# Kernel optimization log

Measured on AMD Instinct MI355X. Metric: run time of the kernel, lower is better.

## Reference

```python
import jax, jax.numpy as jnp
import numpy as np

N_WIRES = 4
DIM = 1 << N_WIRES  # 16
N_PATCH = 14 * 14   # 196


def _random_unitary_16(seed=0):
    # Deterministic surrogate for tq.RandomLayer(n_ops=8): a fixed random
    # real orthogonal 16x16 operator applied to the 4-qubit state.
    rng = np.random.default_rng(seed)
    q, _ = np.linalg.qr(rng.standard_normal((DIM, DIM)))
    return jnp.asarray(q, dtype=jnp.float32)


def _linear_params(rng, fan_in, fan_out):
    bound = 1.0 / np.sqrt(fan_in)
    w = rng.uniform(-bound, bound, size=(fan_out, fan_in)).astype(np.float32)
    b = rng.uniform(-bound, bound, size=(fan_out,)).astype(np.float32)
    return jnp.asarray(w), jnp.asarray(b)


def setup_inputs() -> dict:
    key = jax.random.key(0)
    x = jax.random.normal(key, (8192, 784), dtype=jnp.float32)
    rng = np.random.default_rng(1)
    fc1_w, fc1_b = _linear_params(rng, 784, 120)
    fc2_w, fc2_b = _linear_params(rng, 120, 84)
    fc3_w, fc3_b = _linear_params(rng, 84, 1)
    return {
        "x": x,
        "U": _random_unitary_16(),
        "fc1_w": fc1_w, "fc1_b": fc1_b,
        "fc2_w": fc2_w, "fc2_b": fc2_b,
        "fc3_w": fc3_w, "fc3_b": fc3_b,
    }


def _quantum_filter(x, U):
    # x: [b, 784] -> 2x2 patches in row-major order, per-patch wire data
    # [x[r,c], x[r,c+1], x[r+1,c], x[r+1,c+1]]
    b = x.shape[0]
    xp = x.reshape(b, 14, 2, 14, 2).transpose(0, 1, 3, 2, 4).reshape(b, N_PATCH, N_WIRES)
    # Encoder: RY(theta_w) on wire w starting from |0000> -> product state
    c = jnp.cos(0.5 * xp)  # [b, p, 4]
    s = jnp.sin(0.5 * xp)
    a = jnp.stack([c, s], axis=-1)  # [b, p, 4, 2] per-wire amplitudes
    psi = jnp.einsum("bpi,bpj,bpk,bpl->bpijkl",
                     a[:, :, 0], a[:, :, 1], a[:, :, 2], a[:, :, 3])
    psi = psi.reshape(b, N_PATCH, DIM)  # wire 0 = most significant bit
    # Fixed random layer (16x16 unitary)
    psi = jnp.einsum("ij,bpj->bpi", U, psi)
    # PauliZ expectation per wire: sum_i |psi_i|^2 * (1 - 2*bit_w(i))
    idx = jnp.arange(DIM)
    bits = (idx[:, None] >> (N_WIRES - 1 - jnp.arange(N_WIRES))) & 1  # [16, 4]
    zsign = (1 - 2 * bits).astype(psi.dtype)
    meas = jnp.einsum("bpi,iw->bpw", psi * psi, zsign)  # [b, p, 4]
    return meas.reshape(b, N_PATCH * N_WIRES)  # [b, 784]


def reference(x, U, fc1_w, fc1_b, fc2_w, fc2_b, fc3_w, fc3_b):
    feats = _quantum_filter(x, U)
    h = jax.nn.relu(feats @ fc1_w.T + fc1_b)
    h = jax.nn.relu(h @ fc2_w.T + fc2_b)
    logits = (h @ fc3_w.T + fc3_b)[:, 0]  # [b], matches inputs.squeeze()
    # = P(|1>) = (1 + sin(theta)) / 2 (analytic, shot-noise-free)
    exp_val = 0.5 * (1.0 + jnp.sin(logits))
    p = jax.nn.sigmoid(exp_val)
    return jnp.concatenate([p, 1.0 - p], axis=-1)  # [2*b], matches torch.cat on 1-D
```

## Files before the change

kernel.cpp:

```cpp
#include <hip/hip_runtime.h>
#include <hip/hip_bf16.h>
#include <math.h>


#define BATCH   8192
#define NPATCH  196
#define KPAD    800

typedef __attribute__((ext_vector_type(8))) short bfrag;
typedef __attribute__((ext_vector_type(4))) float f32x4;

static __device__ __forceinline__ unsigned short f2bf(float f) {
    __hip_bfloat16 h = __float2bfloat16(f);
    return __builtin_bit_cast(unsigned short, h);
}

__global__ __launch_bounds__(256) void qfilter_kernel(
    const float* __restrict__ x, const float* __restrict__ U,
    unsigned short* __restrict__ featsB)
{
    int gid = blockIdx.x * 256 + threadIdx.x;
    if (gid >= BATCH * NPATCH) return;
    int b = gid / NPATCH;
    int p = gid - b * NPATCH;
    int pr = p / 14;
    int pc = p - pr * 14;
    const float* xr = x + b * 784 + pr * 56 + pc * 2;
    float x0 = xr[0], x1 = xr[1], x2 = xr[28], x3 = xr[29];

    float s0, c0, s1, c1, s2, c2, s3, c3;
    __sincosf(0.5f * x0, &s0, &c0);
    __sincosf(0.5f * x1, &s1, &c1);
    __sincosf(0.5f * x2, &s2, &c2);
    __sincosf(0.5f * x3, &s3, &c3);

    float t01[4] = {c0 * c1, c0 * s1, s0 * c1, s0 * s1};
    float t23[4] = {c2 * c3, c2 * s3, s2 * c3, s2 * s3};
    float psi[16];
#pragma unroll
    for (int i = 0; i < 16; ++i) psi[i] = t01[i >> 2] * t23[i & 3];

    float m0 = 0.f, m1 = 0.f, m2 = 0.f, m3 = 0.f;
#pragma unroll
    for (int i = 0; i < 16; ++i) {
        float acc = 0.f;
#pragma unroll
        for (int j = 0; j < 16; ++j)
            acc = fmaf(U[i * 16 + j], psi[j], acc);
        float q = acc * acc;
        m0 += (i & 8) ? -q : q;
        m1 += (i & 4) ? -q : q;
        m2 += (i & 2) ? -q : q;
        m3 += (i & 1) ? -q : q;
    }
    ushort4 o;
    o.x = f2bf(m0); o.y = f2bf(m1); o.z = f2bf(m2); o.w = f2bf(m3);
    *reinterpret_cast<ushort4*>(featsB + (size_t)b * KPAD + p * 4) = o;

    if (p == 0) {
        uint4 z = {0u, 0u, 0u, 0u};
        *reinterpret_cast<uint4*>(featsB + (size_t)b * KPAD + 784) = z;
        *reinterpret_cast<uint4*>(featsB + (size_t)b * KPAD + 792) = z;
    }
}

__global__ __launch_bounds__(256) void w1prep_kernel(
    const float* __restrict__ w1, unsigned short* __restrict__ w1B)
{
    int t = blockIdx.x * 256 + threadIdx.x;
    if (t >= 128 * KPAD) return;
    int n = t / KPAD;
    int k = t - n * KPAD;
    float v = (n < 120 && k < 784) ? w1[n * 784 + k] : 0.f;
    w1B[t] = f2bf(v);
}

__global__ __launch_bounds__(64) void fc1_mfma_kernel(
    const unsigned short* __restrict__ featsB,
    const unsigned short* __restrict__ w1B,
    const float* __restrict__ b1, float* __restrict__ h1)
{
    int bid = blockIdx.x;
    int swz = (bid & 7) * 128 + (bid >> 3);
    int m0  = (swz >> 1) * 16;
    int nh  = swz & 1;
    int l   = threadIdx.x;
    int row = l & 15;
    int grp = l >> 4;

    const unsigned short* aptr = featsB + (size_t)(m0 + row) * KPAD + grp * 8;
    const unsigned short* bptr = w1B + (size_t)(nh * 64 + row) * KPAD + grp * 8;

    f32x4 acc0 = {}, acc1 = {}, acc2 = {}, acc3 = {};
    for (int k0 = 0; k0 < KPAD; k0 += 32) {
        bfrag a = *reinterpret_cast<const bfrag*>(aptr + k0);
        bfrag b0 = *reinterpret_cast<const bfrag*>(bptr + 0 * 16 * KPAD + k0);
        bfrag b1f = *reinterpret_cast<const bfrag*>(bptr + 1 * 16 * KPAD + k0);
        bfrag b2 = *reinterpret_cast<const bfrag*>(bptr + 2 * 16 * KPAD + k0);
        bfrag b3 = *reinterpret_cast<const bfrag*>(bptr + 3 * 16 * KPAD + k0);
        acc0 = __builtin_amdgcn_mfma_f32_16x16x32_bf16(a, b0, acc0, 0, 0, 0);
        acc1 = __builtin_amdgcn_mfma_f32_16x16x32_bf16(a, b1f, acc1, 0, 0, 0);
        acc2 = __builtin_amdgcn_mfma_f32_16x16x32_bf16(a, b2, acc2, 0, 0, 0);
        acc3 = __builtin_amdgcn_mfma_f32_16x16x32_bf16(a, b3, acc3, 0, 0, 0);
    }

    f32x4 accs[4] = {acc0, acc1, acc2, acc3};
#pragma unroll
    for (int nj = 0; nj < 4; ++nj) {
        int col = nh * 64 + nj * 16 + row;
        if (col < 120) {
            float bias = b1[col];
#pragma unroll
            for (int r = 0; r < 4; ++r) {
                float v = accs[nj][r] + bias;
                h1[(size_t)(m0 + grp * 4 + r) * 120 + col] = fmaxf(v, 0.f);
            }
        }
    }
}

__global__ __launch_bounds__(256) void head_kernel(
    const float* __restrict__ h1, const float* __restrict__ w2,
    const float* __restrict__ b2, const float* __restrict__ w3,
    const float* __restrict__ b3, float* __restrict__ out)
{
    __shared__ float h1s[64 * 120];
    __shared__ float w2s[84 * 120];
    __shared__ float h2s[64 * 84];
    const int tid = threadIdx.x;
    const int m0  = blockIdx.x * 64;

    for (int t = tid; t < 1920; t += 256) {
        *reinterpret_cast<float4*>(&h1s[t * 4]) =
            *reinterpret_cast<const float4*>(h1 + (size_t)m0 * 120 + t * 4);
    }
    for (int t = tid; t < 2520; t += 256) {
        *reinterpret_cast<float4*>(&w2s[t * 4]) =
            *reinterpret_cast<const float4*>(w2 + t * 4);
    }
    __syncthreads();

    for (int e = tid; e < 1344; e += 256) {
        int r  = e / 21;
        int nq = e - r * 21;
        int n0 = nq * 4;
        float4 bias = *reinterpret_cast<const float4*>(b2 + n0);
        float accv[4] = {bias.x, bias.y, bias.z, bias.w};
#pragma unroll
        for (int kq = 0; kq < 30; ++kq) {
            float4 a = *reinterpret_cast<const float4*>(&h1s[r * 120 + kq * 4]);
#pragma unroll
            for (int nn = 0; nn < 4; ++nn) {
                float4 wv = *reinterpret_cast<const float4*>(
                    &w2s[(n0 + nn) * 120 + kq * 4]);
                accv[nn] = fmaf(a.x, wv.x, accv[nn]);
                accv[nn] = fmaf(a.y, wv.y, accv[nn]);
                accv[nn] = fmaf(a.z, wv.z, accv[nn]);
                accv[nn] = fmaf(a.w, wv.w, accv[nn]);
            }
        }
        float4 o;
        o.x = fmaxf(accv[0], 0.f);
        o.y = fmaxf(accv[1], 0.f);
        o.z = fmaxf(accv[2], 0.f);
        o.w = fmaxf(accv[3], 0.f);
        *reinterpret_cast<float4*>(&h2s[r * 84 + n0]) = o;
    }
    __syncthreads();

    if (tid < 64) {
        int r = tid;
        float acc = b3[0];
#pragma unroll
        for (int kq = 0; kq < 21; ++kq) {
            float4 a  = *reinterpret_cast<const float4*>(&h2s[r * 84 + kq * 4]);
            float4 wv = *reinterpret_cast<const float4*>(w3 + kq * 4);
            acc = fmaf(a.x, wv.x, acc);
            acc = fmaf(a.y, wv.y, acc);
            acc = fmaf(a.z, wv.z, acc);
            acc = fmaf(a.w, wv.w, acc);
        }
        float ev = 0.5f * (1.0f + __sinf(acc));
        float pp = 1.0f / (1.0f + __expf(-ev));
        out[m0 + r]        = pp;
        out[8192 + m0 + r] = 1.0f - pp;
    }
}

extern "C" void kernel_launch(void* const* d_in, const int* in_sizes, int n_in,
                              void* d_out, int out_size, void* d_ws, size_t ws_size,
                              hipStream_t stream)
{
    (void)in_sizes; (void)n_in; (void)out_size; (void)ws_size;
    const float* x  = (const float*)d_in[0];
    const float* U  = (const float*)d_in[1];
    const float* w1 = (const float*)d_in[2];
    const float* b1 = (const float*)d_in[3];
    const float* w2 = (const float*)d_in[4];
    const float* b2 = (const float*)d_in[5];
    const float* w3 = (const float*)d_in[6];
    const float* b3 = (const float*)d_in[7];
    float* out = (float*)d_out;

    unsigned short* featsB = (unsigned short*)d_ws;
    unsigned short* w1B = featsB + (size_t)BATCH * KPAD;
    float* h1 = (float*)(w1B + (size_t)128 * KPAD);

    w1prep_kernel<<<dim3((128 * KPAD + 255) / 256), dim3(256), 0, stream>>>(w1, w1B);
    qfilter_kernel<<<dim3((BATCH * NPATCH) / 256), dim3(256), 0, stream>>>(x, U, featsB);
    fc1_mfma_kernel<<<dim3(1024), dim3(64), 0, stream>>>(featsB, w1B, b1, h1);
    head_kernel<<<dim3(BATCH / 64), dim3(256), 0, stream>>>(h1, w2, b2, w3, b3, out);
}
```

Measured before the change: 143.0 us.

## Fuse quantum filter, fc1 MFMA and head into one per-16-row kernel

Merges the quantum filter, the fc1 MFMA GEMM and the fc2/fc3 head into a single kernel in which each block handles 16 batch rows and keeps the bf16 features and h1 in shared memory. This removes the global round-trips for featsB and h1 and two kernel launches. The filter math is rewritten with float2 packed operations and a butterfly-style reduction for the Z expectations. In exchange, w2 is now read from global memory or cache inside the inner loop instead of being staged in LDS, and fc1 uses only two MFMA tiles per wave over a small 16-row M tile.

```diff
diff --git a/kernel.cpp b/kernel.cpp
--- a/kernel.cpp
+++ b/kernel.cpp
@@ -6,62 +6,16 @@
 #define BATCH   8192
 #define NPATCH  196
 #define KPAD    800
+#define FLD     808
+#define H1LD    132
 
 typedef __attribute__((ext_vector_type(8))) short bfrag;
 typedef __attribute__((ext_vector_type(4))) float f32x4;
+typedef __attribute__((ext_vector_type(2))) float f32x2;
 
 static __device__ __forceinline__ unsigned short f2bf(float f) {
     __hip_bfloat16 h = __float2bfloat16(f);
     return __builtin_bit_cast(unsigned short, h);
-}
-
-__global__ __launch_bounds__(256) void qfilter_kernel(
-    const float* __restrict__ x, const float* __restrict__ U,
-    unsigned short* __restrict__ featsB)
-{
-    int gid = blockIdx.x * 256 + threadIdx.x;
-    if (gid >= BATCH * NPATCH) return;
-    int b = gid / NPATCH;
-    int p = gid - b * NPATCH;
-    int pr = p / 14;
-    int pc = p - pr * 14;
-    const float* xr = x + b * 784 + pr * 56 + pc * 2;
-    float x0 = xr[0], x1 = xr[1], x2 = xr[28], x3 = xr[29];
-
-    float s0, c0, s1, c1, s2, c2, s3, c3;
-    __sincosf(0.5f * x0, &s0, &c0);
-    __sincosf(0.5f * x1, &s1, &c1);
-    __sincosf(0.5f * x2, &s2, &c2);
-    __sincosf(0.5f * x3, &s3, &c3);
-
-    float t01[4] = {c0 * c1, c0 * s1, s0 * c1, s0 * s1};
-    float t23[4] = {c2 * c3, c2 * s3, s2 * c3, s2 * s3};
-    float psi[16];
-#pragma unroll
-    for (int i = 0; i < 16; ++i) psi[i] = t01[i >> 2] * t23[i & 3];
-
-    float m0 = 0.f, m1 = 0.f, m2 = 0.f, m3 = 0.f;
-#pragma unroll
-    for (int i = 0; i < 16; ++i) {
-        float acc = 0.f;
-#pragma unroll
-        for (int j = 0; j < 16; ++j)
-            acc = fmaf(U[i * 16 + j], psi[j], acc);
-        float q = acc * acc;
-        m0 += (i & 8) ? -q : q;
-        m1 += (i & 4) ? -q : q;
-        m2 += (i & 2) ? -q : q;
-        m3 += (i & 1) ? -q : q;
-    }
-    ushort4 o;
-    o.x = f2bf(m0); o.y = f2bf(m1); o.z = f2bf(m2); o.w = f2bf(m3);
-    *reinterpret_cast<ushort4*>(featsB + (size_t)b * KPAD + p * 4) = o;
-
-    if (p == 0) {
-        uint4 z = {0u, 0u, 0u, 0u};
-        *reinterpret_cast<uint4*>(featsB + (size_t)b * KPAD + 784) = z;
-        *reinterpret_cast<uint4*>(featsB + (size_t)b * KPAD + 792) = z;
-    }
 }
 
 __global__ __launch_bounds__(256) void w1prep_kernel(
@@ -75,72 +29,123 @@
     w1B[t] = f2bf(v);
 }
 
-__global__ __launch_bounds__(64) void fc1_mfma_kernel(
-    const unsigned short* __restrict__ featsB,
+__global__ __launch_bounds__(256) void mega_kernel(
+    const float* __restrict__ x, const float* __restrict__ U,
     const unsigned short* __restrict__ w1B,
-    const float* __restrict__ b1, float* __restrict__ h1)
+    const float* __restrict__ b1,
+    const float* __restrict__ w2, const float* __restrict__ b2,
+    const float* __restrict__ w3, const float* __restrict__ b3,
+    float* __restrict__ out)
 {
-    int bid = blockIdx.x;
-    int swz = (bid & 7) * 128 + (bid >> 3);
-    int m0  = (swz >> 1) * 16;
-    int nh  = swz & 1;
-    int l   = threadIdx.x;
-    int row = l & 15;
-    int grp = l >> 4;
-
-    const unsigned short* aptr = featsB + (size_t)(m0 + row) * KPAD + grp * 8;
-    const unsigned short* bptr = w1B + (size_t)(nh * 64 + row) * KPAD + grp * 8;
-
-    f32x4 acc0 = {}, acc1 = {}, acc2 = {}, acc3 = {};
-    for (int k0 = 0; k0 < KPAD; k0 += 32) {
-        bfrag a = *reinterpret_cast<const bfrag*>(aptr + k0);
-        bfrag b0 = *reinterpret_cast<const bfrag*>(bptr + 0 * 16 * KPAD + k0);
-        bfrag b1f = *reinterpret_cast<const bfrag*>(bptr + 1 * 16 * KPAD + k0);
-        bfrag b2 = *reinterpret_cast<const bfrag*>(bptr + 2 * 16 * KPAD + k0);
-        bfrag b3 = *reinterpret_cast<const bfrag*>(bptr + 3 * 16 * KPAD + k0);
-        acc0 = __builtin_amdgcn_mfma_f32_16x16x32_bf16(a, b0, acc0, 0, 0, 0);
-        acc1 = __builtin_amdgcn_mfma_f32_16x16x32_bf16(a, b1f, acc1, 0, 0, 0);
-        acc2 = __builtin_amdgcn_mfma_f32_16x16x32_bf16(a, b2, acc2, 0, 0, 0);
-        acc3 = __builtin_amdgcn_mfma_f32_16x16x32_bf16(a, b3, acc3, 0, 0, 0);
-    }
-
-    f32x4 accs[4] = {acc0, acc1, acc2, acc3};
-#pragma unroll
-    for (int nj = 0; nj < 4; ++nj) {
-        int col = nh * 64 + nj * 16 + row;
-        if (col < 120) {
-            float bias = b1[col];
-#pragma unroll
-            for (int r = 0; r < 4; ++r) {
-                float v = accs[nj][r] + bias;
-                h1[(size_t)(m0 + grp * 4 + r) * 120 + col] = fmaxf(v, 0.f);
+    __shared__ unsigned short featsL[16 * FLD];
+    __shared__ float h1L[16 * H1LD];
+    __shared__ float h2L[16 * 84];
+
+    const int tid = threadIdx.x;
+    const int m0  = blockIdx.x * 16;
+
+    {
+        int r = tid >> 4;
+        int c = 784 + (tid & 15);
+        featsL[r * FLD + c] = 0;
+    }
+
+    const f32x2* U2 = reinterpret_cast<const f32x2*>(U);
+    for (int e = tid; e < 16 * NPATCH; e += 256) {
+        int r = e / NPATCH;
+        int p = e - r * NPATCH;
+        int pr = p / 14;
+        int pc = p - pr * 14;
+        const float* xr = x + (size_t)(m0 + r) * 784 + pr * 56 + pc * 2;
+        f32x2 xa = *reinterpret_cast<const f32x2*>(xr);
+        f32x2 xb = *reinterpret_cast<const f32x2*>(xr + 28);
+
+        float s0, c0, s1, c1, s2, c2, s3, c3;
+        __sincosf(0.5f * xa.x, &s0, &c0);
+        __sincosf(0.5f * xa.y, &s1, &c1);
+        __sincosf(0.5f * xb.x, &s2, &c2);
+        __sincosf(0.5f * xb.y, &s3, &c3);
+
+        float t01[4] = {c0 * c1, c0 * s1, s0 * c1, s0 * s1};
+        f32x2 t23p0 = {c2 * c3, c2 * s3};
+        f32x2 t23p1 = {s2 * c3, s2 * s3};
+
+        f32x2 psi2[8];
+#pragma unroll
+        for (int j = 0; j < 8; ++j)
+            psi2[j] = ((j & 1) ? t23p1 : t23p0) * t01[j >> 1];
+
+        f32x2 q2[8];
+#pragma unroll
+        for (int jq = 0; jq < 8; ++jq) {
+            f32x2 accA = U2[(2 * jq) * 8] * psi2[0];
+            f32x2 accB = U2[(2 * jq + 1) * 8] * psi2[0];
+#pragma unroll
+            for (int j = 1; j < 8; ++j) {
+                accA = U2[(2 * jq) * 8 + j] * psi2[j] + accA;
+                accB = U2[(2 * jq + 1) * 8 + j] * psi2[j] + accB;
             }
-        }
-    }
-}
-
-__global__ __launch_bounds__(256) void head_kernel(
-    const float* __restrict__ h1, const float* __restrict__ w2,
-    const float* __restrict__ b2, const float* __restrict__ w3,
-    const float* __restrict__ b3, float* __restrict__ out)
-{
-    __shared__ float h1s[64 * 120];
-    __shared__ float w2s[84 * 120];
-    __shared__ float h2s[64 * 84];
-    const int tid = threadIdx.x;
-    const int m0  = blockIdx.x * 64;
-
-    for (int t = tid; t < 1920; t += 256) {
-        *reinterpret_cast<float4*>(&h1s[t * 4]) =
-            *reinterpret_cast<const float4*>(h1 + (size_t)m0 * 120 + t * 4);
-    }
-    for (int t = tid; t < 2520; t += 256) {
-        *reinterpret_cast<float4*>(&w2s[t * 4]) =
-            *reinterpret_cast<const float4*>(w2 + t * 4);
+            float pa = accA.x + accA.y;
+            float pb = accB.x + accB.y;
+            f32x2 ph = {pa, pb};
+            q2[jq] = ph * ph;
+        }
+
+        f32x2 s01 = q2[0] + q2[1], s23 = q2[2] + q2[3];
+        f32x2 s45 = q2[4] + q2[5], s67 = q2[6] + q2[7];
+        f32x2 e0 = s01 + s23, e1 = s45 + s67;
+        f32x2 t0 = s01 - s23, t1 = s45 - s67;
+        f32x2 g  = (q2[0] - q2[1]) + (q2[2] - q2[3])
+                 + (q2[4] - q2[5]) + (q2[6] - q2[7]);
+        f32x2 F  = e0 + e1;
+        float m0v = (e0.x + e0.y) - (e1.x + e1.y);
+        float m1v = (t0.x + t0.y) + (t1.x + t1.y);
+        float m2v = g.x + g.y;
+        float m3v = F.x - F.y;
+
+        ushort4 o;
+        o.x = f2bf(m0v); o.y = f2bf(m1v); o.z = f2bf(m2v); o.w = f2bf(m3v);
+        *reinterpret_cast<ushort4*>(&featsL[r * FLD + p * 4]) = o;
     }
     __syncthreads();
 
-    for (int e = tid; e < 1344; e += 256) {
+    {
+        const int wave = tid >> 6;
+        const int lane = tid & 63;
+        const int row  = lane & 15;
+        const int grp  = lane >> 4;
+
+        const unsigned short* fA = &featsL[row * FLD + grp * 8];
+        const unsigned short* bp0 =
+            w1B + (size_t)(wave * 32 + row) * KPAD + grp * 8;
+        const unsigned short* bp1 = bp0 + 16 * KPAD;
+
+        f32x4 acc0 = {}, acc1 = {};
+        for (int k0 = 0; k0 < KPAD; k0 += 32) {
+            bfrag a  = *reinterpret_cast<const bfrag*>(fA + k0);
+            bfrag b0 = *reinterpret_cast<const bfrag*>(bp0 + k0);
+            bfrag b1f = *reinterpret_cast<const bfrag*>(bp1 + k0);
+            acc0 = __builtin_amdgcn_mfma_f32_16x16x32_bf16(a, b0, acc0, 0, 0, 0);
+            acc1 = __builtin_amdgcn_mfma_f32_16x16x32_bf16(a, b1f, acc1, 0, 0, 0);
+        }
+
+        f32x4 accs[2] = {acc0, acc1};
+#pragma unroll
+        for (int nj = 0; nj < 2; ++nj) {
+            int col = wave * 32 + nj * 16 + row;
+            if (col < 120) {
+                float bias = b1[col];
+#pragma unroll
+                for (int rr = 0; rr < 4; ++rr) {
+                    float v = accs[nj][rr] + bias;
+                    h1L[(grp * 4 + rr) * H1LD + col] = fmaxf(v, 0.f);
+                }
+            }
+        }
+    }
+    __syncthreads();
+
+    for (int e = tid; e < 16 * 21; e += 256) {
         int r  = e / 21;
         int nq = e - r * 21;
         int n0 = nq * 4;
@@ -148,11 +153,11 @@
         float accv[4] = {bias.x, bias.y, bias.z, bias.w};
 #pragma unroll
         for (int kq = 0; kq < 30; ++kq) {
-            float4 a = *reinterpret_cast<const float4*>(&h1s[r * 120 + kq * 4]);
+            float4 a = *reinterpret_cast<const float4*>(&h1L[r * H1LD + kq * 4]);
 #pragma unroll
             for (int nn = 0; nn < 4; ++nn) {
-                float4 wv = *reinterpret_cast<const float4*>(
-                    &w2s[(n0 + nn) * 120 + kq * 4]);
+                const float4 wv = *reinterpret_cast<const float4*>(
+                    w2 + (size_t)(n0 + nn) * 120 + kq * 4);
                 accv[nn] = fmaf(a.x, wv.x, accv[nn]);
                 accv[nn] = fmaf(a.y, wv.y, accv[nn]);
                 accv[nn] = fmaf(a.z, wv.z, accv[nn]);
@@ -164,16 +169,16 @@
         o.y = fmaxf(accv[1], 0.f);
         o.z = fmaxf(accv[2], 0.f);
         o.w = fmaxf(accv[3], 0.f);
-        *reinterpret_cast<float4*>(&h2s[r * 84 + n0]) = o;
+        *reinterpret_cast<float4*>(&h2L[r * 84 + n0]) = o;
     }
     __syncthreads();
 
-    if (tid < 64) {
+    if (tid < 16) {
         int r = tid;
         float acc = b3[0];
 #pragma unroll
         for (int kq = 0; kq < 21; ++kq) {
-            float4 a  = *reinterpret_cast<const float4*>(&h2s[r * 84 + kq * 4]);
+            float4 a  = *reinterpret_cast<const float4*>(&h2L[r * 84 + kq * 4]);
             float4 wv = *reinterpret_cast<const float4*>(w3 + kq * 4);
             acc = fmaf(a.x, wv.x, acc);
             acc = fmaf(a.y, wv.y, acc);
@@ -182,8 +187,8 @@
         }
         float ev = 0.5f * (1.0f + __sinf(acc));
         float pp = 1.0f / (1.0f + __expf(-ev));
-        out[m0 + r]        = pp;
-        out[8192 + m0 + r] = 1.0f - pp;
+        out[m0 + r]         = pp;
+        out[BATCH + m0 + r] = 1.0f - pp;
     }
 }
 
@@ -202,12 +207,9 @@
     const float* b3 = (const float*)d_in[7];
     float* out = (float*)d_out;
 
-    unsigned short* featsB = (unsigned short*)d_ws;
-    unsigned short* w1B = featsB + (size_t)BATCH * KPAD;
-    float* h1 = (float*)(w1B + (size_t)128 * KPAD);
+    unsigned short* w1B = (unsigned short*)d_ws;
 
     w1prep_kernel<<<dim3((128 * KPAD + 255) / 256), dim3(256), 0, stream>>>(w1, w1B);
-    qfilter_kernel<<<dim3((BATCH * NPATCH) / 256), dim3(256), 0, stream>>>(x, U, featsB);
-    fc1_mfma_kernel<<<dim3(1024), dim3(64), 0, stream>>>(featsB, w1B, b1, h1);
-    head_kernel<<<dim3(BATCH / 64), dim3(256), 0, stream>>>(h1, w2, b2, w3, b3, out);
-}
+    mega_kernel<<<dim3(BATCH / 16), dim3(256), 0, stream>>>(
+        x, U, w1B, b1, w2, b2, w3, b3, out);
+}
```

Measured after the change: 191.1 us. +33.6%, slower.
